# Kernel tuning notes

Hardware: AMD Instinct MI355X
Metric: run time of the kernel (lower is better)

## Reference

```python
import jax, jax.numpy as jnp
import numpy as np


def setup_inputs() -> dict:
    key = jax.random.key(0)
    x = jax.random.normal(key, (32, 256, 128, 128), dtype=jnp.float32)
    return {"x": x}


def reference(x):
    b, c, h, w = x.shape
    # global average pool over spatial dims, per (b, c)
    pooled = jnp.mean(x, axis=(2, 3), keepdims=True)          # [b, c, 1, 1]
    # xn = (x * pooled).mean over channels -> [b, 1, h, w]
    xn = jnp.mean(x * pooled, axis=1, keepdims=True)
    # mean over batch -> [h, w]
    entro = jnp.mean(xn, axis=0)[0]
    e = entro.reshape(-1)
    emin = jnp.min(e)
    emax = jnp.max(e)
    e = (e - emin) / (emax - emin) * 255.0
    # torch.histc(bins=256, min=0, max=255): 256 uniform bins, last bin
    # right-inclusive -> matches jnp.histogram semantics.
    his, _ = jnp.histogram(e, bins=256, range=(0.0, 255.0))
    his = jax.lax.stop_gradient(his.astype(x.dtype)) / (h * w)
    entro_final = jnp.sum(his * -jnp.log(his + 1e-8))
    nz = jnp.count_nonzero(his).astype(x.dtype)
    entro_final = entro_final / nz
    s = jnp.mean(jax.nn.sigmoid(xn))
    return s + entro_final * 10.0
```

## Files before the change

kernel.cpp:

```cpp
#include <hip/hip_runtime.h>
#include <math.h>

#define BB 32
#define CC 256
#define HW 16384
#define BC (BB*CC)


__global__ __launch_bounds__(256) void pool_kernel(const float* __restrict__ x,
                                                   float* __restrict__ ws) {
    const int bc = blockIdx.x;
    const int t  = threadIdx.x;
    const float4* xv = (const float4*)x + (size_t)bc * (HW / 4);
    float s = 0.f;
#pragma unroll
    for (int i = 0; i < 16; ++i) {
        float4 v = xv[t + i * 256];
        s += v.x + v.y + v.z + v.w;
    }
    for (int o = 32; o > 0; o >>= 1) s += __shfl_down(s, o);
    __shared__ float part[4];
    if ((t & 63) == 0) part[t >> 6] = s;
    __syncthreads();
    if (t == 0) {
        float tot = part[0] + part[1] + part[2] + part[3];
        ws[bc] = tot * (1.0f / HW);
    }
    int tid = bc * 256 + t;
    if (tid < HW) ws[BC + tid] = 0.f;
    if (tid == 0) ws[BC + HW] = 0.f;
}

__global__ __launch_bounds__(256) void xn_kernel(const float* __restrict__ x,
                                                 float* __restrict__ ws) {
    const int b     = blockIdx.x >> 4;
    const int chunk = blockIdx.x & 15;
    const int t     = threadIdx.x;

    __shared__ float spool[CC];
    spool[t] = ws[b * CC + t];
    __syncthreads();

    const float4* xv = (const float4*)x;
    const size_t base = (size_t)b * CC * (HW / 4) + (size_t)chunk * 256 + t;

    float ax = 0.f, ay = 0.f, az = 0.f, aw = 0.f;
#pragma unroll 4
    for (int c = 0; c < CC; ++c) {
        float4 v = xv[base + (size_t)c * (HW / 4)];
        float p = spool[c];
        ax += v.x * p; ay += v.y * p; az += v.z * p; aw += v.w * p;
    }
    const float inv_c = 1.0f / CC;
    float xn0 = ax * inv_c, xn1 = ay * inv_c, xn2 = az * inv_c, xn3 = aw * inv_c;

    float* entro = ws + BC;
    const int hw = (chunk * 256 + t) * 4;
    const float inv_b = 1.0f / BB;
    atomicAdd(&entro[hw + 0], xn0 * inv_b);
    atomicAdd(&entro[hw + 1], xn1 * inv_b);
    atomicAdd(&entro[hw + 2], xn2 * inv_b);
    atomicAdd(&entro[hw + 3], xn3 * inv_b);

    float sg = 1.f / (1.f + expf(-xn0)) + 1.f / (1.f + expf(-xn1)) +
               1.f / (1.f + expf(-xn2)) + 1.f / (1.f + expf(-xn3));
    for (int o = 32; o > 0; o >>= 1) sg += __shfl_down(sg, o);
    __shared__ float part[4];
    if ((t & 63) == 0) part[t >> 6] = sg;
    __syncthreads();
    if (t == 0) {
        float tot = part[0] + part[1] + part[2] + part[3];
        atomicAdd(&ws[BC + HW], tot);
    }
}

__global__ __launch_bounds__(256) void finalize_kernel(const float* __restrict__ ws,
                                                       float* __restrict__ out) {
    const int t = threadIdx.x;
    const float* entro = ws + BC;

    float lmin = INFINITY, lmax = -INFINITY;
#pragma unroll
    for (int i = 0; i < 64; ++i) {
        float v = entro[t + i * 256];
        lmin = fminf(lmin, v);
        lmax = fmaxf(lmax, v);
    }
    for (int o = 32; o > 0; o >>= 1) {
        lmin = fminf(lmin, __shfl_down(lmin, o));
        lmax = fmaxf(lmax, __shfl_down(lmax, o));
    }
    __shared__ float smin[4], smax[4];
    __shared__ float bmin, bmax;
    if ((t & 63) == 0) { smin[t >> 6] = lmin; smax[t >> 6] = lmax; }
    __syncthreads();
    if (t == 0) {
        bmin = fminf(fminf(smin[0], smin[1]), fminf(smin[2], smin[3]));
        bmax = fmaxf(fmaxf(smax[0], smax[1]), fmaxf(smax[2], smax[3]));
    }
    __shared__ unsigned int hist[256];
    hist[t] = 0u;
    __syncthreads();

    const float emin = bmin, emax = bmax;
    const float scale = 256.0f / (emax - emin);
#pragma unroll
    for (int i = 0; i < 64; ++i) {
        float v = entro[t + i * 256];
        int idx = (int)floorf((v - emin) * scale);
        idx = idx < 0 ? 0 : (idx > 255 ? 255 : idx);
        atomicAdd(&hist[idx], 1u);
    }
    __syncthreads();

    const unsigned int h = hist[t];
    const float his = (float)h * (1.0f / HW);
    float term = (h > 0u) ? his * (-logf(his + 1e-8f)) : 0.f;
    float nzf  = (h > 0u) ? 1.f : 0.f;
    for (int o = 32; o > 0; o >>= 1) {
        term += __shfl_down(term, o);
        nzf  += __shfl_down(nzf, o);
    }
    __shared__ float sterm[4], snz[4];
    if ((t & 63) == 0) { sterm[t >> 6] = term; snz[t >> 6] = nzf; }
    __syncthreads();
    if (t == 0) {
        float ent = sterm[0] + sterm[1] + sterm[2] + sterm[3];
        float nz  = snz[0] + snz[1] + snz[2] + snz[3];
        float sig = ws[BC + HW] * (1.0f / ((float)BB * (float)HW));
        out[0] = sig + (ent / nz) * 10.0f;
    }
}

extern "C" void kernel_launch(void* const* d_in, const int* in_sizes, int n_in,
                              void* d_out, int out_size, void* d_ws, size_t ws_size,
                              hipStream_t stream) {
    const float* x = (const float*)d_in[0];
    float* out = (float*)d_out;
    float* ws  = (float*)d_ws;

    pool_kernel<<<BC, 256, 0, stream>>>(x, ws);
    xn_kernel<<<BB * 16, 256, 0, stream>>>(x, ws);
    finalize_kernel<<<1, 256, 0, stream>>>(ws, out);
}
```

Measured before the change: 766.7 us.

## Split channel reduction across more blocks and add separate partial-sum reduce kernel

The xn pass splits the 256 channels into four groups, launching four times as many blocks. Each block writes partial dot-products to workspace instead of atomically accumulating into entro. A new reduce kernel sums the channel-group partials over batch, producing entro and the sigmoid sum without per-element atomics. This raises occupancy for the main streaming pass, at the cost of an extra 8MB write/read and one more launch.

After: 785.5 us. 2.4% more time.

```diff
diff --git a/kernel.cpp b/kernel.cpp
--- a/kernel.cpp
+++ b/kernel.cpp
@@ -6,6 +6,10 @@
 #define HW 16384
 #define BC (BB*CC)
 
+#define WS_POOLED 0
+#define WS_PART   8192
+#define WS_ENTRO  (8192 + 4*BB*HW)
+#define WS_SIG    (WS_ENTRO + HW)
 
 __global__ __launch_bounds__(256) void pool_kernel(const float* __restrict__ x,
                                                    float* __restrict__ ws) {
@@ -24,60 +28,73 @@
     __syncthreads();
     if (t == 0) {
         float tot = part[0] + part[1] + part[2] + part[3];
-        ws[bc] = tot * (1.0f / HW);
+        ws[WS_POOLED + bc] = tot * (1.0f / HW);
+        if (bc == 0) ws[WS_SIG] = 0.f;
     }
-    int tid = bc * 256 + t;
-    if (tid < HW) ws[BC + tid] = 0.f;
-    if (tid == 0) ws[BC + HW] = 0.f;
 }
 
 __global__ __launch_bounds__(256) void xn_kernel(const float* __restrict__ x,
                                                  float* __restrict__ ws) {
-    const int b     = blockIdx.x >> 4;
-    const int chunk = blockIdx.x & 15;
+    const int bx    = blockIdx.x;
+    const int b     = bx >> 6;
+    const int rem   = bx & 63;
+    const int chunk = rem >> 2;
+    const int cg    = rem & 3;
     const int t     = threadIdx.x;
 
-    __shared__ float spool[CC];
-    spool[t] = ws[b * CC + t];
+    __shared__ float spool[64];
+    if (t < 64) spool[t] = ws[WS_POOLED + b * CC + cg * 64 + t];
     __syncthreads();
 
     const float4* xv = (const float4*)x;
-    const size_t base = (size_t)b * CC * (HW / 4) + (size_t)chunk * 256 + t;
+    const size_t base = (size_t)b * CC * (HW / 4) +
+                        (size_t)(cg * 64) * (HW / 4) +
+                        (size_t)chunk * 256 + t;
 
     float ax = 0.f, ay = 0.f, az = 0.f, aw = 0.f;
 #pragma unroll 4
-    for (int c = 0; c < CC; ++c) {
+    for (int c = 0; c < 64; ++c) {
         float4 v = xv[base + (size_t)c * (HW / 4)];
         float p = spool[c];
         ax += v.x * p; ay += v.y * p; az += v.z * p; aw += v.w * p;
     }
+
+    float4* partv = (float4*)(ws + WS_PART);
+    partv[(size_t)(cg * BB + b) * (HW / 4) + chunk * 256 + t] =
+        make_float4(ax, ay, az, aw);
+}
+
+__global__ __launch_bounds__(256) void reduce_kernel(float* __restrict__ ws) {
+    const int hw = blockIdx.x * 256 + threadIdx.x;
+    const int t  = threadIdx.x;
+    const float* part = ws + WS_PART;
+
+    float ent = 0.f, sg = 0.f;
     const float inv_c = 1.0f / CC;
-    float xn0 = ax * inv_c, xn1 = ay * inv_c, xn2 = az * inv_c, xn3 = aw * inv_c;
+#pragma unroll
+    for (int b = 0; b < BB; ++b) {
+        float s = 0.f;
+#pragma unroll
+        for (int g = 0; g < 4; ++g)
+            s += part[(size_t)(g * BB + b) * HW + hw];
+        float xnb = s * inv_c;
+        ent += xnb;
+        sg  += 1.f / (1.f + expf(-xnb));
+    }
+    ws[WS_ENTRO + hw] = ent * (1.0f / BB);
 
-    float* entro = ws + BC;
-    const int hw = (chunk * 256 + t) * 4;
-    const float inv_b = 1.0f / BB;
-    atomicAdd(&entro[hw + 0], xn0 * inv_b);
-    atomicAdd(&entro[hw + 1], xn1 * inv_b);
-    atomicAdd(&entro[hw + 2], xn2 * inv_b);
-    atomicAdd(&entro[hw + 3], xn3 * inv_b);
-
-    float sg = 1.f / (1.f + expf(-xn0)) + 1.f / (1.f + expf(-xn1)) +
-               1.f / (1.f + expf(-xn2)) + 1.f / (1.f + expf(-xn3));
     for (int o = 32; o > 0; o >>= 1) sg += __shfl_down(sg, o);
-    __shared__ float part[4];
-    if ((t & 63) == 0) part[t >> 6] = sg;
+    __shared__ float partl[4];
+    if ((t & 63) == 0) partl[t >> 6] = sg;
     __syncthreads();
-    if (t == 0) {
-        float tot = part[0] + part[1] + part[2] + part[3];
-        atomicAdd(&ws[BC + HW], tot);
-    }
+    if (t == 0)
+        atomicAdd(&ws[WS_SIG], partl[0] + partl[1] + partl[2] + partl[3]);
 }
 
 __global__ __launch_bounds__(256) void finalize_kernel(const float* __restrict__ ws,
                                                        float* __restrict__ out) {
     const int t = threadIdx.x;
-    const float* entro = ws + BC;
+    const float* entro = ws + WS_ENTRO;
 
     float lmin = INFINITY, lmax = -INFINITY;
 #pragma unroll
@@ -127,7 +144,7 @@
     if (t == 0) {
         float ent = sterm[0] + sterm[1] + sterm[2] + sterm[3];
         float nz  = snz[0] + snz[1] + snz[2] + snz[3];
-        float sig = ws[BC + HW] * (1.0f / ((float)BB * (float)HW));
+        float sig = ws[WS_SIG] * (1.0f / ((float)BB * (float)HW));
         out[0] = sig + (ent / nz) * 10.0f;
     }
 }
@@ -140,6 +157,7 @@
     float* ws  = (float*)d_ws;
 
     pool_kernel<<<BC, 256, 0, stream>>>(x, ws);
-    xn_kernel<<<BB * 16, 256, 0, stream>>>(x, ws);
+    xn_kernel<<<BB * 16 * 4, 256, 0, stream>>>(x, ws);
+    reduce_kernel<<<HW / 256, 256, 0, stream>>>(ws);
     finalize_kernel<<<1, 256, 0, stream>>>(ws, out);
 }
```
